# Kernel tuning notes

Hardware: AMD Instinct MI355X
Metric: run time of the kernel (lower is better)

## Reference

```python
import jax, jax.numpy as jnp
import numpy as np

N = 50000      # nodes
E = 800000     # edges (before self-loops)
F_IN = 128     # num_node_features
H = 128        # hidden_channels
G = 256        # graphs in batch
T = 4          # num_tasks


def setup_inputs() -> dict:
    key = jax.random.key(0)
    ks = jax.random.split(key, 12)
    x = jax.random.normal(ks[0], (N, F_IN), jnp.float32)
    edge_index = jax.random.randint(ks[1], (2, E), 0, N, dtype=jnp.int64)
    batch = jnp.sort(jax.random.randint(ks[2], (N,), 0, G, dtype=jnp.int64))
    s_in = 1.0 / np.sqrt(F_IN)
    s_h = 1.0 / np.sqrt(H)
    W1 = jax.random.normal(ks[3], (F_IN, H), jnp.float32) * s_in
    b1 = jnp.zeros((H,), jnp.float32)
    W2 = jax.random.normal(ks[4], (H, H), jnp.float32) * s_h
    b2 = jnp.zeros((H,), jnp.float32)
    Wfc = jax.random.normal(ks[5], (H, H), jnp.float32) * s_h
    bfc = jnp.zeros((H,), jnp.float32)
    Wh = jax.random.normal(ks[6], (T, H, 2), jnp.float32) * s_h
    bh = jnp.zeros((T, 2), jnp.float32)
    return {"x": x, "edge_index": edge_index, "batch": batch,
            "W1": W1, "b1": b1, "W2": W2, "b2": b2,
            "Wfc": Wfc, "bfc": bfc, "Wh": Wh, "bh": bh}


def _gcn_layer(x, W, b, src, dst, dinv):
    # GCNConv: out = D^{-1/2}(A+I)D^{-1/2} X W + b  (self-loops already in src/dst)
    h = x @ W                                    # [N, H] dense transform first (fewer edge features)
    coef = dinv[src] * dinv[dst]                 # [E+N] symmetric normalization
    msg = h[src] * coef[:, None]                 # [E+N, H] gathered messages
    out = jax.ops.segment_sum(msg, dst, num_segments=N)
    return out + b


def reference(x, edge_index, batch, W1, b1, W2, b2, Wfc, bfc, Wh, bh):
    loops = jnp.arange(N, dtype=edge_index.dtype)
    src = jnp.concatenate([edge_index[0], loops])  # [E+N]
    dst = jnp.concatenate([edge_index[1], loops])
    deg = jax.ops.segment_sum(jnp.ones_like(dst, dtype=x.dtype), dst, num_segments=N)
    dinv = jax.lax.rsqrt(deg)                      # deg >= 1 due to self-loops

    h = jax.nn.relu(_gcn_layer(x, W1, b1, src, dst, dinv))
    h = jax.nn.relu(_gcn_layer(h, W2, b2, src, dst, dinv))

    # global_mean_pool over batch ids
    sums = jax.ops.segment_sum(h, batch, num_segments=G)          # [G, H]
    cnt = jax.ops.segment_sum(jnp.ones((N,), h.dtype), batch, num_segments=G)
    pooled = sums / jnp.maximum(cnt, 1.0)[:, None]

    z = jax.nn.relu(pooled @ Wfc + bfc)                           # [G, H]
    out = jnp.einsum('gh,thc->tgc', z, Wh) + bh[:, None, :]       # [T, G, 2]
    return out
```

## Files before the change

### kernel.cpp

```cpp
#include <hip/hip_runtime.h>
#include <math.h>

constexpr int N = 50000;
constexpr int E = 800000;
constexpr int F = 128;
constexpr int G = 256;
constexpr int T = 4;

constexpr int BSH   = 5;
constexpr int BNODES= 1 << BSH;
constexpr int NBUCK = (N + BNODES - 1) / BNODES;
constexpr int CHUNK = 2048;
constexpr int NCHUNK= (E + CHUNK - 1) / CHUNK;
constexpr int SSH   = 13;

constexpr int WC_BLKS  = (F * F + 255) / 256;
constexpr int PRE_H0   = 2 * WC_BLKS;
constexpr int PRE_BLKS = PRE_H0 + NCHUNK;

constexpr int GB1 = (N + 63) / 64;
constexpr int AGB = N / 16;

typedef __attribute__((ext_vector_type(8))) short short8;
typedef __attribute__((ext_vector_type(4))) float floatx4;

__device__ inline float bf2f(unsigned short u) {
    union { unsigned int i; float f; } v;
    v.i = ((unsigned int)u) << 16;
    return v.f;
}
__device__ inline unsigned short f2bf(float f) {
    union { float f; unsigned int i; } v;
    v.f = f;
    unsigned int r = v.i + 0x7FFF + ((v.i >> 16) & 1);
    return (unsigned short)(r >> 16);
}
__device__ inline unsigned int pack2bf(float a, float b) {
    return (unsigned int)f2bf(a) | ((unsigned int)f2bf(b) << 16);
}

__device__ inline void wcast_one(const float* __restrict__ W,
                                 unsigned short* __restrict__ Whi,
                                 unsigned short* __restrict__ Wlo, int i) {
    if (i >= F * F) return;
    int k = i >> 7, n = i & 127;
    float w = W[i];
    unsigned short hi = f2bf(w);
    unsigned short lo = f2bf(w - bf2f(hi));
    int s = k >> 5, q = (k >> 3) & 3, j = k & 7;
    int idx = (((s * 128 + n) * 4 + q) * 8) + j;
    Whi[idx] = hi;
    Wlo[idx] = lo;
}

__global__ __launch_bounds__(256) void k_pre(const float* __restrict__ W1, const float* __restrict__ W2,
                                             unsigned short* __restrict__ w1h, unsigned short* __restrict__ w1l,
                                             unsigned short* __restrict__ w2h, unsigned short* __restrict__ w2l,
                                             const int* __restrict__ dst, int* __restrict__ cnts) {
    __shared__ int h[NBUCK];
    int b = blockIdx.x, t = threadIdx.x;
    if (b < WC_BLKS) {
        wcast_one(W1, w1h, w1l, b * 256 + t);
    } else if (b < 2 * WC_BLKS) {
        wcast_one(W2, w2h, w2l, (b - WC_BLKS) * 256 + t);
    } else {
        int chunk = b - PRE_H0;
        for (int i = t; i < NBUCK; i += 256) h[i] = 0;
        __syncthreads();
        int base = chunk * CHUNK;
        for (int i = t; i < CHUNK; i += 256) {
            int e = base + i;
            if (e < E) atomicAdd(&h[dst[e] >> BSH], 1);
        }
        __syncthreads();
        for (int i = t; i < NBUCK; i += 256) cnts[chunk * NBUCK + i] = h[i];
    }
}

__global__ __launch_bounds__(256) void k_colscan(int* __restrict__ cnts, int* __restrict__ btot) {
    int j = blockIdx.x * 256 + threadIdx.x;
    if (j >= NBUCK) return;
    int run = 0;
    for (int k = 0; k < NCHUNK; ++k) {
        int v = cnts[k * NBUCK + j];
        cnts[k * NBUCK + j] = run;
        run += v;
    }
    btot[j] = run;
}

__global__ __launch_bounds__(256) void k_bucketscan(const int* __restrict__ btot,
                                                    int* __restrict__ bucketbase) {
    __shared__ int part[256];
    int t = threadIdx.x;
    constexpr int CH = (NBUCK + 255) / 256;
    int beg = t * CH;
    int end = (beg + CH < NBUCK) ? beg + CH : NBUCK;
    int tot[CH];
    int s = 0;
    for (int i = beg; i < end; ++i) {
        tot[i - beg] = btot[i];
        s += btot[i];
    }
    part[t] = s;
    __syncthreads();
    for (int off = 1; off < 256; off <<= 1) {
        int u = (t >= off) ? part[t - off] : 0;
        __syncthreads();
        part[t] += u;
        __syncthreads();
    }
    int run = (t == 0) ? 0 : part[t - 1];
    for (int i = beg; i < end; ++i) {
        bucketbase[i] = run;
        run += tot[i - beg];
    }
    if (t == 255) bucketbase[NBUCK] = part[255];
}

__global__ __launch_bounds__(256) void k_fillb(const int* __restrict__ src,
                                               const int* __restrict__ dst,
                                               const int* __restrict__ cnts,
                                               const int* __restrict__ bucketbase,
                                               unsigned int* __restrict__ staging) {
    __shared__ int lofs[NBUCK];
    int chunk = blockIdx.x, t = threadIdx.x;
    for (int i = t; i < NBUCK; i += 256)
        lofs[i] = bucketbase[i] + cnts[chunk * NBUCK + i];
    __syncthreads();
    int base = chunk * CHUNK;
    for (int i = t; i < CHUNK; i += 256) {
        int e = base + i;
        if (e < E) {
            int d = dst[e];
            int pos = atomicAdd(&lofs[d >> BSH], 1);
            staging[pos] = (unsigned int)src[e] | ((unsigned int)(d & (BNODES - 1)) << 16);
        }
    }
}

__global__ __launch_bounds__(256) void k_passB(const unsigned int* __restrict__ staging,
                                               const int* __restrict__ bucketbase,
                                               int* __restrict__ csr,
                                               int* __restrict__ rowstart,
                                               float* __restrict__ dinv) {
    __shared__ unsigned int ent[1024];
    __shared__ int h[BNODES * 8], off_a[BNODES * 8];
    __shared__ int nodebase[BNODES], ndeg[BNODES];
    int b = blockIdx.x, t = threadIdx.x;
    int jb = bucketbase[b], je = bucketbase[b + 1];
    int M = je - jb;
    if (M > 1024) M = 1024;
    if (t < BNODES * 8) h[t] = 0;
    __syncthreads();

    for (int i = t; i < M; i += 256) {
        unsigned int en = staging[jb + i];
        ent[i] = en;
        int key = (((en >> 16) & (BNODES - 1)) << 3) | ((en & 0xFFFFu) >> SSH);
        atomicAdd(&h[key], 1);
    }
    __syncthreads();

    if (t < BNODES) {
        int s = 0;
#pragma unroll
        for (int c = 0; c < 8; ++c) s += h[t * 8 + c];
        ndeg[t] = s;
    }
    __syncthreads();
    if (t == 0) {
        int run = jb;
        for (int k = 0; k < BNODES; ++k) {
            nodebase[k] = run;
            run += ndeg[k];
        }
    }
    __syncthreads();
    if (t < BNODES) {
        int run = nodebase[t];
#pragma unroll
        for (int c = 0; c < 8; ++c) {
            off_a[t * 8 + c] = run;
            run += h[t * 8 + c];
        }
        int node = b * BNODES + t;
        if (node < N) {
            rowstart[node] = nodebase[t];
            dinv[node] = rsqrtf((float)(ndeg[t] + 1));
        }
    }
    if (b == 0 && t == 0) rowstart[N] = E;
    __syncthreads();

    for (int i = t; i < M; i += 256) {
        unsigned int en = ent[i];
        int key = (((en >> 16) & (BNODES - 1)) << 3) | ((en & 0xFFFFu) >> SSH);
        int loc = atomicAdd(&off_a[key], 1);
        csr[loc] = (int)(en & 0xFFFFu);
    }
}

template <bool ABF16>
__device__ __forceinline__ void gemm_body(const void* __restrict__ Ain,
                                          const unsigned short* __restrict__ Wph,
                                          const unsigned short* __restrict__ Wpl,
                                          const float* __restrict__ dinv,
                                          unsigned short* __restrict__ C16,
                                          int row0, int tid) {
    __shared__ __align__(16) unsigned short Albs[64 * 136];

    if (ABF16) {
        const uint4* A8 = (const uint4*)Ain;
        for (int f = tid; f < 64 * 16; f += 256) {
            int r = f >> 4, kq = f & 15;
            int row = row0 + r;
            uint4 v = make_uint4(0u, 0u, 0u, 0u);
            if (row < N) v = A8[row * 16 + kq];
            *(uint4*)&Albs[r * 136 + kq * 8] = v;
        }
    } else {
        const float4* A4 = (const float4*)Ain;
        for (int f = tid; f < 64 * 32; f += 256) {
            int r = f >> 5, kq = f & 31;
            int row = row0 + r;
            float4 v = make_float4(0.f, 0.f, 0.f, 0.f);
            if (row < N) v = A4[row * 32 + kq];
            ushort4 o;
            o.x = f2bf(v.x); o.y = f2bf(v.y); o.z = f2bf(v.z); o.w = f2bf(v.w);
            *(ushort4*)&Albs[r * 136 + kq * 4] = o;
        }
    }
    __syncthreads();

    int wv = tid >> 6;
    int lane = tid & 63;
    int c16 = lane & 15;
    int q = lane >> 4;
    int m = wv * 16 + c16;

    floatx4 acc[8];
#pragma unroll
    for (int nt = 0; nt < 8; ++nt) acc[nt] = (floatx4){0.f, 0.f, 0.f, 0.f};

    const short8* WH = (const short8*)Wph;
    const short8* WL = (const short8*)Wpl;
#pragma unroll
    for (int s = 0; s < 4; ++s) {
        short8 a = *(const short8*)&Albs[m * 136 + s * 32 + q * 8];
        int wb = s * 512 + c16 * 4 + q;
#pragma unroll
        for (int nt = 0; nt < 8; ++nt) {
            acc[nt] = __builtin_amdgcn_mfma_f32_16x16x32_bf16(a, WH[wb + nt * 64], acc[nt], 0, 0, 0);
            acc[nt] = __builtin_amdgcn_mfma_f32_16x16x32_bf16(a, WL[wb + nt * 64], acc[nt], 0, 0, 0);
        }
    }

    int rbase = row0 + wv * 16 + q * 4;
#pragma unroll
    for (int r = 0; r < 4; ++r) {
        int row = rbase + r;
        if (row < N) {
            float dv = dinv[row];
#pragma unroll
            for (int nt = 0; nt < 8; ++nt)
                C16[row * 128 + nt * 16 + c16] = f2bf(acc[nt][r] * dv);
        }
    }
}

template <bool ABF16>
__global__ __launch_bounds__(256) void k_gemm(const void* __restrict__ Ain,
                                              const unsigned short* __restrict__ Wph,
                                              const unsigned short* __restrict__ Wpl,
                                              const float* __restrict__ dinv,
                                              unsigned short* __restrict__ C16) {
    gemm_body<ABF16>(Ain, Wph, Wpl, dinv, C16, blockIdx.x * 64, threadIdx.x);
}

__device__ inline void fma8(const uint4& u, float c, float* acc) {
    union { unsigned int i; float f; } a;
    a.i = u.x << 16;          acc[0] = fmaf(a.f, c, acc[0]);
    a.i = u.x & 0xFFFF0000u;  acc[1] = fmaf(a.f, c, acc[1]);
    a.i = u.y << 16;          acc[2] = fmaf(a.f, c, acc[2]);
    a.i = u.y & 0xFFFF0000u;  acc[3] = fmaf(a.f, c, acc[3]);
    a.i = u.z << 16;          acc[4] = fmaf(a.f, c, acc[4]);
    a.i = u.z & 0xFFFF0000u;  acc[5] = fmaf(a.f, c, acc[5]);
    a.i = u.w << 16;          acc[6] = fmaf(a.f, c, acc[6]);
    a.i = u.w & 0xFFFF0000u;  acc[7] = fmaf(a.f, c, acc[7]);
}

__device__ __forceinline__ void agg_loop(const uint4* __restrict__ t8,
                                         const int* __restrict__ csr,
                                         int jb, int je, int lane, float* acc) {
    for (int j = jb; j < je; j += 8) {
        int e[8];
        float msk[8];
#pragma unroll
        for (int k = 0; k < 8; ++k) {
            int idx = j + k;
            e[k] = csr[idx < je ? idx : je - 1];
            msk[k] = (idx < je) ? 1.0f : 0.0f;
        }
        uint4 u[8];
#pragma unroll
        for (int k = 0; k < 8; ++k) u[k] = t8[e[k] * 16 + lane];
#pragma unroll
        for (int k = 0; k < 8; ++k) fma8(u[k], msk[k], acc);
    }
}

__global__ __launch_bounds__(256) void k_agg1gemm(const unsigned short* __restrict__ tmp16,
                                                  const int* __restrict__ csr,
                                                  const int* __restrict__ rowstart,
                                                  const float* __restrict__ dinv,
                                                  const float* __restrict__ bias,
                                                  const unsigned short* __restrict__ w2h,
                                                  const unsigned short* __restrict__ w2l,
                                                  unsigned short* __restrict__ tmp2) {
    __shared__ __align__(16) unsigned short Albs[16 * 136];
    int tid = threadIdx.x;
    int row0 = blockIdx.x * 16;

    {
        int node = row0 + (tid >> 4);
        int lane = tid & 15;
        const uint4* t8 = (const uint4*)tmp16;
        float acc[8] = {0.f, 0.f, 0.f, 0.f, 0.f, 0.f, 0.f, 0.f};
        fma8(t8[node * 16 + lane], 1.0f, acc);
        agg_loop(t8, csr, rowstart[node], rowstart[node + 1], lane, acc);

        float di = dinv[node];
        const float4* b4 = (const float4*)bias;
        float4 ba = b4[lane * 2], bb = b4[lane * 2 + 1];
        uint4 o;
        o.x = pack2bf(fmaxf(fmaf(acc[0], di, ba.x), 0.f), fmaxf(fmaf(acc[1], di, ba.y), 0.f));
        o.y = pack2bf(fmaxf(fmaf(acc[2], di, ba.z), 0.f), fmaxf(fmaf(acc[3], di, ba.w), 0.f));
        o.z = pack2bf(fmaxf(fmaf(acc[4], di, bb.x), 0.f), fmaxf(fmaf(acc[5], di, bb.y), 0.f));
        o.w = pack2bf(fmaxf(fmaf(acc[6], di, bb.z), 0.f), fmaxf(fmaf(acc[7], di, bb.w), 0.f));
        *(uint4*)&Albs[(tid >> 4) * 136 + lane * 8] = o;
    }
    __syncthreads();

    int wv = tid >> 6;
    int lane = tid & 63;
    int c16 = lane & 15;
    int q = lane >> 4;

    floatx4 acc[2];
    acc[0] = (floatx4){0.f, 0.f, 0.f, 0.f};
    acc[1] = (floatx4){0.f, 0.f, 0.f, 0.f};

    const short8* WH = (const short8*)w2h;
    const short8* WL = (const short8*)w2l;
#pragma unroll
    for (int s = 0; s < 4; ++s) {
        short8 a = *(const short8*)&Albs[c16 * 136 + s * 32 + q * 8];
        int wb = s * 512 + c16 * 4 + q;
#pragma unroll
        for (int i = 0; i < 2; ++i) {
            int nt = wv * 2 + i;
            acc[i] = __builtin_amdgcn_mfma_f32_16x16x32_bf16(a, WH[wb + nt * 64], acc[i], 0, 0, 0);
            acc[i] = __builtin_amdgcn_mfma_f32_16x16x32_bf16(a, WL[wb + nt * 64], acc[i], 0, 0, 0);
        }
    }

    int rbase = row0 + q * 4;
#pragma unroll
    for (int r = 0; r < 4; ++r) {
        int row = rbase + r;
        float dv = dinv[row];
#pragma unroll
        for (int i = 0; i < 2; ++i) {
            int nt = wv * 2 + i;
            tmp2[row * 128 + nt * 16 + c16] = f2bf(acc[i][r] * dv);
        }
    }
}

__global__ __launch_bounds__(256) void k_agg(const unsigned short* __restrict__ tmp16,
                                             const int* __restrict__ csr,
                                             const int* __restrict__ rowstart,
                                             const float* __restrict__ dinv,
                                             const float* __restrict__ bias,
                                             unsigned short* __restrict__ out16) {
    int node = (blockIdx.x * blockDim.x + threadIdx.x) >> 4;
    int lane = threadIdx.x & 15;
    if (node >= N) return;
    const uint4* t8 = (const uint4*)tmp16;
    float acc[8] = {0.f, 0.f, 0.f, 0.f, 0.f, 0.f, 0.f, 0.f};
    fma8(t8[node * 16 + lane], 1.0f, acc);
    agg_loop(t8, csr, rowstart[node], rowstart[node + 1], lane, acc);

    float di = dinv[node];
    const float4* b4 = (const float4*)bias;
    float4 ba = b4[lane * 2], bb = b4[lane * 2 + 1];
    uint4 o;
    o.x = pack2bf(fmaxf(fmaf(acc[0], di, ba.x), 0.f), fmaxf(fmaf(acc[1], di, ba.y), 0.f));
    o.y = pack2bf(fmaxf(fmaf(acc[2], di, ba.z), 0.f), fmaxf(fmaf(acc[3], di, ba.w), 0.f));
    o.z = pack2bf(fmaxf(fmaf(acc[4], di, bb.x), 0.f), fmaxf(fmaf(acc[5], di, bb.y), 0.f));
    o.w = pack2bf(fmaxf(fmaf(acc[6], di, bb.z), 0.f), fmaxf(fmaf(acc[7], di, bb.w), 0.f));
    ((uint4*)out16)[node * 16 + lane] = o;
}

__global__ __launch_bounds__(256) void k_poolhead(const unsigned short* __restrict__ h16,
                                                  const int* __restrict__ batch,
                                                  const float* __restrict__ Wfc,
                                                  const float* __restrict__ bfc,
                                                  const float* __restrict__ Wh,
                                                  const float* __restrict__ bh,
                                                  float* __restrict__ out) {
    __shared__ float red[16][128];
    __shared__ float p[128];
    __shared__ float zs[128];
    int g = blockIdx.x, t = threadIdx.x;
    int rg = t >> 4, lane = t & 15;

    int lo = 0, hi = N;
    while (lo < hi) { int m = (lo + hi) >> 1; if (batch[m] < g) lo = m + 1; else hi = m; }
    int lo1 = lo, hi1 = N;
    while (lo1 < hi1) { int m = (lo1 + hi1) >> 1; if (batch[m] < g + 1) lo1 = m + 1; else hi1 = m; }
    int cnt = lo1 - lo;

    float acc[8] = {0.f, 0.f, 0.f, 0.f, 0.f, 0.f, 0.f, 0.f};
    const uint4* h4 = (const uint4*)h16;
    for (int i = lo + rg; i < lo1; i += 16)
        fma8(h4[i * 16 + lane], 1.0f, acc);
#pragma unroll
    for (int k = 0; k < 8; ++k) red[rg][lane * 8 + k] = acc[k];
    __syncthreads();

    if (t < 128) {
        float s = 0.f;
#pragma unroll
        for (int r = 0; r < 16; ++r) s += red[r][t];
        p[t] = s / (float)((cnt > 1) ? cnt : 1);
    }
    __syncthreads();

    if (t < 128) {
        float a = bfc[t];
        for (int k = 0; k < F; ++k) a = fmaf(p[k], Wfc[k * F + t], a);
        zs[t] = fmaxf(a, 0.f);
    }
    __syncthreads();

    if (t < T * 2) {
        int task = t >> 1, c = t & 1;
        float a = bh[task * 2 + c];
        const float* wr = &Wh[task * F * 2 + c];
        for (int h = 0; h < F; ++h) a = fmaf(zs[h], wr[h * 2], a);
        out[task * (G * 2) + g * 2 + c] = a;
    }
}

extern "C" void kernel_launch(void* const* d_in, const int* in_sizes, int n_in,
                              void* d_out, int out_size, void* d_ws, size_t ws_size,
                              hipStream_t stream) {
    const float* x    = (const float*)d_in[0];
    const int*   ei   = (const int*)d_in[1];
    const int*   batch= (const int*)d_in[2];
    const float* W1   = (const float*)d_in[3];
    const float* b1   = (const float*)d_in[4];
    const float* W2   = (const float*)d_in[5];
    const float* b2   = (const float*)d_in[6];
    const float* Wfc  = (const float*)d_in[7];
    const float* bfc  = (const float*)d_in[8];
    const float* Wh   = (const float*)d_in[9];
    const float* bh   = (const float*)d_in[10];
    float* out = (float*)d_out;

    const int* srcp = ei;
    const int* dstp = ei + E;

    char* w = (char*)d_ws;
    auto alloc = [&](size_t bytes) {
        char* p = w;
        w += (bytes + 255) & ~(size_t)255;
        return p;
    };
    unsigned short* tmp16 = (unsigned short*)alloc((size_t)N * F * 2);
    unsigned short* tmp2  = (unsigned short*)alloc((size_t)N * F * 2);
    unsigned short* hbuf16= (unsigned short*)alloc((size_t)N * F * 2);
    int*   csr      = (int*)  alloc((size_t)E * 4);
    unsigned int* staging = (unsigned int*)alloc((size_t)E * 4);
    int*   cnts     = (int*)  alloc((size_t)NCHUNK * NBUCK * 4);
    int*   btot     = (int*)  alloc((size_t)NBUCK * 4);
    int*   bucketbase=(int*)  alloc((size_t)(NBUCK + 1) * 4);
    int*   rowstart = (int*)  alloc((size_t)(N + 1) * 4);
    float* dinv     = (float*)alloc((size_t)N * 4);
    unsigned short* w1h = (unsigned short*)alloc((size_t)F * F * 2);
    unsigned short* w1l = (unsigned short*)alloc((size_t)F * F * 2);
    unsigned short* w2h = (unsigned short*)alloc((size_t)F * F * 2);
    unsigned short* w2l = (unsigned short*)alloc((size_t)F * F * 2);

    k_pre<<<PRE_BLKS, 256, 0, stream>>>(W1, W2, w1h, w1l, w2h, w2l, dstp, cnts);

    k_colscan<<<(NBUCK + 255) / 256, 256, 0, stream>>>(cnts, btot);
    k_bucketscan<<<1, 256, 0, stream>>>(btot, bucketbase);
    k_fillb<<<NCHUNK, 256, 0, stream>>>(srcp, dstp, cnts, bucketbase, staging);
    k_passB<<<NBUCK, 256, 0, stream>>>(staging, bucketbase, csr, rowstart, dinv);

    k_gemm<false><<<GB1, 256, 0, stream>>>(x, w1h, w1l, dinv, tmp16);

    k_agg1gemm<<<AGB, 256, 0, stream>>>(tmp16, csr, rowstart, dinv, b1, w2h, w2l, tmp2);

    k_agg<<<(N * 16 + 255) / 256, 256, 0, stream>>>(tmp2, csr, rowstart, dinv, b2, hbuf16);

    k_poolhead<<<G, 256, 0, stream>>>(hbuf16, batch, Wfc, bfc, Wh, bh, out);
}
```

Baseline: 246.6 us.

## Fuse mean-pool into aggregation, merge column scan with first GEMM, per-edge dinv

Removes the dinv scaling from the GEMM epilogues and instead applies dinv[src] per edge inside the aggregation loop. This lets the first GEMM run before the CSR build, so it is merged with a parallel per-bucket column scan into one launch. The second aggregation now pools directly into a zeroed G×F buffer via shared-memory run-length reduction and atomics, which eliminates the hbuf16 write and re-read and one kernel launch. The trade-off is an extra per-edge dinv gather and float atomics that make summation order nondeterministic.

```diff
diff --git a/kernel.cpp b/kernel.cpp
--- a/kernel.cpp
+++ b/kernel.cpp
@@ -15,10 +15,13 @@
 constexpr int SSH   = 13;
 
 constexpr int WC_BLKS  = (F * F + 255) / 256;
-constexpr int PRE_H0   = 2 * WC_BLKS;
+constexpr int PRE_Z0   = 2 * WC_BLKS;
+constexpr int PRE_ZB   = (G * F + 255) / 256;
+constexpr int PRE_H0   = PRE_Z0 + PRE_ZB;
 constexpr int PRE_BLKS = PRE_H0 + NCHUNK;
 
 constexpr int GB1 = (N + 63) / 64;
+constexpr int GCB = GB1 + NBUCK;
 constexpr int AGB = N / 16;
 
 typedef __attribute__((ext_vector_type(8))) short short8;
@@ -56,13 +59,16 @@
 __global__ __launch_bounds__(256) void k_pre(const float* __restrict__ W1, const float* __restrict__ W2,
                                              unsigned short* __restrict__ w1h, unsigned short* __restrict__ w1l,
                                              unsigned short* __restrict__ w2h, unsigned short* __restrict__ w2l,
-                                             const int* __restrict__ dst, int* __restrict__ cnts) {
+                                             const int* __restrict__ dst, int* __restrict__ cnts,
+                                             float* __restrict__ pooled) {
     __shared__ int h[NBUCK];
     int b = blockIdx.x, t = threadIdx.x;
     if (b < WC_BLKS) {
         wcast_one(W1, w1h, w1l, b * 256 + t);
     } else if (b < 2 * WC_BLKS) {
         wcast_one(W2, w2h, w2l, (b - WC_BLKS) * 256 + t);
+    } else if (b < PRE_H0) {
+        pooled[(b - PRE_Z0) * 256 + t] = 0.f;
     } else {
         int chunk = b - PRE_H0;
         for (int i = t; i < NBUCK; i += 256) h[i] = 0;
@@ -75,18 +81,6 @@
         __syncthreads();
         for (int i = t; i < NBUCK; i += 256) cnts[chunk * NBUCK + i] = h[i];
     }
-}
-
-__global__ __launch_bounds__(256) void k_colscan(int* __restrict__ cnts, int* __restrict__ btot) {
-    int j = blockIdx.x * 256 + threadIdx.x;
-    if (j >= NBUCK) return;
-    int run = 0;
-    for (int k = 0; k < NCHUNK; ++k) {
-        int v = cnts[k * NBUCK + j];
-        cnts[k * NBUCK + j] = run;
-        run += v;
-    }
-    btot[j] = run;
 }
 
 __global__ __launch_bounds__(256) void k_bucketscan(const int* __restrict__ btot,
@@ -205,11 +199,9 @@
 __device__ __forceinline__ void gemm_body(const void* __restrict__ Ain,
                                           const unsigned short* __restrict__ Wph,
                                           const unsigned short* __restrict__ Wpl,
-                                          const float* __restrict__ dinv,
                                           unsigned short* __restrict__ C16,
-                                          int row0, int tid) {
-    __shared__ __align__(16) unsigned short Albs[64 * 136];
-
+                                          int row0, int tid,
+                                          unsigned short* __restrict__ Albs) {
     if (ABF16) {
         const uint4* A8 = (const uint4*)Ain;
         for (int f = tid; f < 64 * 16; f += 256) {
@@ -261,21 +253,43 @@
     for (int r = 0; r < 4; ++r) {
         int row = rbase + r;
         if (row < N) {
-            float dv = dinv[row];
 #pragma unroll
             for (int nt = 0; nt < 8; ++nt)
-                C16[row * 128 + nt * 16 + c16] = f2bf(acc[nt][r] * dv);
-        }
-    }
-}
-
-template <bool ABF16>
-__global__ __launch_bounds__(256) void k_gemm(const void* __restrict__ Ain,
-                                              const unsigned short* __restrict__ Wph,
-                                              const unsigned short* __restrict__ Wpl,
-                                              const float* __restrict__ dinv,
-                                              unsigned short* __restrict__ C16) {
-    gemm_body<ABF16>(Ain, Wph, Wpl, dinv, C16, blockIdx.x * 64, threadIdx.x);
+                C16[row * 128 + nt * 16 + c16] = f2bf(acc[nt][r]);
+        }
+    }
+}
+
+__global__ __launch_bounds__(256) void k_gemmcol(const float* __restrict__ x,
+                                                 const unsigned short* __restrict__ w1h,
+                                                 const unsigned short* __restrict__ w1l,
+                                                 unsigned short* __restrict__ tmp16,
+                                                 int* __restrict__ cnts,
+                                                 int* __restrict__ btot) {
+    __shared__ __align__(16) unsigned short Albs[64 * 136];
+    int b = blockIdx.x, t = threadIdx.x;
+    if (b < GB1) {
+        gemm_body<false>(x, w1h, w1l, tmp16, b * 64, t, Albs);
+        return;
+    }
+    int j = b - GB1;
+    int* part = (int*)Albs;
+    int k0 = 2 * t, k1 = 2 * t + 1;
+    int v0 = (k0 < NCHUNK) ? cnts[k0 * NBUCK + j] : 0;
+    int v1 = (k1 < NCHUNK) ? cnts[k1 * NBUCK + j] : 0;
+    int s = v0 + v1;
+    part[t] = s;
+    __syncthreads();
+    for (int off = 1; off < 256; off <<= 1) {
+        int u = (t >= off) ? part[t - off] : 0;
+        __syncthreads();
+        part[t] += u;
+        __syncthreads();
+    }
+    int excl = part[t] - s;
+    if (k0 < NCHUNK) cnts[k0 * NBUCK + j] = excl;
+    if (k1 < NCHUNK) cnts[k1 * NBUCK + j] = excl + v0;
+    if (t == 255) btot[j] = part[255];
 }
 
 __device__ inline void fma8(const uint4& u, float c, float* acc) {
@@ -292,21 +306,22 @@
 
 __device__ __forceinline__ void agg_loop(const uint4* __restrict__ t8,
                                          const int* __restrict__ csr,
+                                         const float* __restrict__ dinv,
                                          int jb, int je, int lane, float* acc) {
     for (int j = jb; j < je; j += 8) {
         int e[8];
-        float msk[8];
+        float cf[8];
 #pragma unroll
         for (int k = 0; k < 8; ++k) {
             int idx = j + k;
             e[k] = csr[idx < je ? idx : je - 1];
-            msk[k] = (idx < je) ? 1.0f : 0.0f;
+            cf[k] = (idx < je) ? dinv[e[k]] : 0.0f;
         }
         uint4 u[8];
 #pragma unroll
         for (int k = 0; k < 8; ++k) u[k] = t8[e[k] * 16 + lane];
 #pragma unroll
-        for (int k = 0; k < 8; ++k) fma8(u[k], msk[k], acc);
+        for (int k = 0; k < 8; ++k) fma8(u[k], cf[k], acc);
     }
 }
 
@@ -326,11 +341,11 @@
         int node = row0 + (tid >> 4);
         int lane = tid & 15;
         const uint4* t8 = (const uint4*)tmp16;
+        float di = dinv[node];
         float acc[8] = {0.f, 0.f, 0.f, 0.f, 0.f, 0.f, 0.f, 0.f};
-        fma8(t8[node * 16 + lane], 1.0f, acc);
-        agg_loop(t8, csr, rowstart[node], rowstart[node + 1], lane, acc);
-
-        float di = dinv[node];
+        fma8(t8[node * 16 + lane], di, acc);
+        agg_loop(t8, csr, dinv, rowstart[node], rowstart[node + 1], lane, acc);
+
         const float4* b4 = (const float4*)bias;
         float4 ba = b4[lane * 2], bb = b4[lane * 2 + 1];
         uint4 o;
@@ -369,11 +384,10 @@
 #pragma unroll
     for (int r = 0; r < 4; ++r) {
         int row = rbase + r;
-        float dv = dinv[row];
 #pragma unroll
         for (int i = 0; i < 2; ++i) {
             int nt = wv * 2 + i;
-            tmp2[row * 128 + nt * 16 + c16] = f2bf(acc[i][r] * dv);
+            tmp2[row * 128 + nt * 16 + c16] = f2bf(acc[i][r]);
         }
     }
 }
@@ -383,74 +397,81 @@
                                              const int* __restrict__ rowstart,
                                              const float* __restrict__ dinv,
                                              const float* __restrict__ bias,
-                                             unsigned short* __restrict__ out16) {
-    int node = (blockIdx.x * blockDim.x + threadIdx.x) >> 4;
-    int lane = threadIdx.x & 15;
-    if (node >= N) return;
+                                             const int* __restrict__ batch,
+                                             float* __restrict__ pooled) {
+    __shared__ float red[16][128];
+    __shared__ int gid[16];
+    int tid = threadIdx.x;
+    int node0 = blockIdx.x * 16;
+    int ns = tid >> 4, lane = tid & 15;
+    int node = node0 + ns;
     const uint4* t8 = (const uint4*)tmp16;
+    float di = dinv[node];
     float acc[8] = {0.f, 0.f, 0.f, 0.f, 0.f, 0.f, 0.f, 0.f};
-    fma8(t8[node * 16 + lane], 1.0f, acc);
-    agg_loop(t8, csr, rowstart[node], rowstart[node + 1], lane, acc);
-
-    float di = dinv[node];
+    fma8(t8[node * 16 + lane], di, acc);
+    agg_loop(t8, csr, dinv, rowstart[node], rowstart[node + 1], lane, acc);
+
     const float4* b4 = (const float4*)bias;
     float4 ba = b4[lane * 2], bb = b4[lane * 2 + 1];
-    uint4 o;
-    o.x = pack2bf(fmaxf(fmaf(acc[0], di, ba.x), 0.f), fmaxf(fmaf(acc[1], di, ba.y), 0.f));
-    o.y = pack2bf(fmaxf(fmaf(acc[2], di, ba.z), 0.f), fmaxf(fmaf(acc[3], di, ba.w), 0.f));
-    o.z = pack2bf(fmaxf(fmaf(acc[4], di, bb.x), 0.f), fmaxf(fmaf(acc[5], di, bb.y), 0.f));
-    o.w = pack2bf(fmaxf(fmaf(acc[6], di, bb.z), 0.f), fmaxf(fmaf(acc[7], di, bb.w), 0.f));
-    ((uint4*)out16)[node * 16 + lane] = o;
-}
-
-__global__ __launch_bounds__(256) void k_poolhead(const unsigned short* __restrict__ h16,
+    red[ns][lane * 8 + 0] = fmaxf(fmaf(acc[0], di, ba.x), 0.f);
+    red[ns][lane * 8 + 1] = fmaxf(fmaf(acc[1], di, ba.y), 0.f);
+    red[ns][lane * 8 + 2] = fmaxf(fmaf(acc[2], di, ba.z), 0.f);
+    red[ns][lane * 8 + 3] = fmaxf(fmaf(acc[3], di, ba.w), 0.f);
+    red[ns][lane * 8 + 4] = fmaxf(fmaf(acc[4], di, bb.x), 0.f);
+    red[ns][lane * 8 + 5] = fmaxf(fmaf(acc[5], di, bb.y), 0.f);
+    red[ns][lane * 8 + 6] = fmaxf(fmaf(acc[6], di, bb.z), 0.f);
+    red[ns][lane * 8 + 7] = fmaxf(fmaf(acc[7], di, bb.w), 0.f);
+    if (tid < 16) gid[tid] = batch[node0 + tid];
+    __syncthreads();
+
+    if (tid < 128) {
+        int f = tid;
+        float run = 0.f;
+        int g = gid[0];
+        for (int r = 0; r < 16; ++r) {
+            if (gid[r] != g) {
+                atomicAdd(&pooled[g * 128 + f], run);
+                run = 0.f;
+                g = gid[r];
+            }
+            run += red[r][f];
+        }
+        atomicAdd(&pooled[g * 128 + f], run);
+    }
+}
+
+__global__ __launch_bounds__(128) void k_poolhead(const float* __restrict__ pooled,
                                                   const int* __restrict__ batch,
                                                   const float* __restrict__ Wfc,
                                                   const float* __restrict__ bfc,
                                                   const float* __restrict__ Wh,
                                                   const float* __restrict__ bh,
                                                   float* __restrict__ out) {
-    __shared__ float red[16][128];
     __shared__ float p[128];
     __shared__ float zs[128];
     int g = blockIdx.x, t = threadIdx.x;
-    int rg = t >> 4, lane = t & 15;
 
     int lo = 0, hi = N;
     while (lo < hi) { int m = (lo + hi) >> 1; if (batch[m] < g) lo = m + 1; else hi = m; }
     int lo1 = lo, hi1 = N;
     while (lo1 < hi1) { int m = (lo1 + hi1) >> 1; if (batch[m] < g + 1) lo1 = m + 1; else hi1 = m; }
     int cnt = lo1 - lo;
-
-    float acc[8] = {0.f, 0.f, 0.f, 0.f, 0.f, 0.f, 0.f, 0.f};
-    const uint4* h4 = (const uint4*)h16;
-    for (int i = lo + rg; i < lo1; i += 16)
-        fma8(h4[i * 16 + lane], 1.0f, acc);
-#pragma unroll
-    for (int k = 0; k < 8; ++k) red[rg][lane * 8 + k] = acc[k];
-    __syncthreads();
-
-    if (t < 128) {
-        float s = 0.f;
-#pragma unroll
-        for (int r = 0; r < 16; ++r) s += red[r][t];
-        p[t] = s / (float)((cnt > 1) ? cnt : 1);
-    }
-    __syncthreads();
-
-    if (t < 128) {
-        float a = bfc[t];
-        for (int k = 0; k < F; ++k) a = fmaf(p[k], Wfc[k * F + t], a);
-        zs[t] = fmaxf(a, 0.f);
-    }
+    float inv = 1.0f / (float)((cnt > 1) ? cnt : 1);
+
+    p[t] = pooled[g * 128 + t] * inv;
+    __syncthreads();
+
+    float a = bfc[t];
+    for (int k = 0; k < F; ++k) a = fmaf(p[k], Wfc[k * F + t], a);
+    zs[t] = fmaxf(a, 0.f);
     __syncthreads();
 
     if (t < T * 2) {
         int task = t >> 1, c = t & 1;
-        float a = bh[task * 2 + c];
+        float a2 = bh[task * 2 + c];
         const float* wr = &Wh[task * F * 2 + c];
-        for (int h = 0; h < F; ++h) a = fmaf(zs[h], wr[h * 2], a);
-        out[task * (G * 2) + g * 2 + c] = a;
+        for (int h = 0; h < F; ++h) a2 = fmaf(zs[h], wr[h * 2], a2);
+        out[task * (G * 2) + g * 2 + c] = a2;
     }
 }
 
@@ -481,7 +502,6 @@
     };
     unsigned short* tmp16 = (unsigned short*)alloc((size_t)N * F * 2);
     unsigned short* tmp2  = (unsigned short*)alloc((size_t)N * F * 2);
-    unsigned short* hbuf16= (unsigned short*)alloc((size_t)N * F * 2);
     int*   csr      = (int*)  alloc((size_t)E * 4);
     unsigned int* staging = (unsigned int*)alloc((size_t)E * 4);
     int*   cnts     = (int*)  alloc((size_t)NCHUNK * NBUCK * 4);
@@ -489,23 +509,23 @@
     int*   bucketbase=(int*)  alloc((size_t)(NBUCK + 1) * 4);
     int*   rowstart = (int*)  alloc((size_t)(N + 1) * 4);
     float* dinv     = (float*)alloc((size_t)N * 4);
+    float* pooled   = (float*)alloc((size_t)G * F * 4);
     unsigned short* w1h = (unsigned short*)alloc((size_t)F * F * 2);
     unsigned short* w1l = (unsigned short*)alloc((size_t)F * F * 2);
     unsigned short* w2h = (unsigned short*)alloc((size_t)F * F * 2);
     unsigned short* w2l = (unsigned short*)alloc((size_t)F * F * 2);
 
-    k_pre<<<PRE_BLKS, 256, 0, stream>>>(W1, W2, w1h, w1l, w2h, w2l, dstp, cnts);
-
-    k_colscan<<<(NBUCK + 255) / 256, 256, 0, stream>>>(cnts, btot);
+    k_pre<<<PRE_BLKS, 256, 0, stream>>>(W1, W2, w1h, w1l, w2h, w2l, dstp, cnts, pooled);
+
+    k_gemmcol<<<GCB, 256, 0, stream>>>(x, w1h, w1l, tmp16, cnts, btot);
+
     k_bucketscan<<<1, 256, 0, stream>>>(btot, bucketbase);
     k_fillb<<<NCHUNK, 256, 0, stream>>>(srcp, dstp, cnts, bucketbase, staging);
     k_passB<<<NBUCK, 256, 0, stream>>>(staging, bucketbase, csr, rowstart, dinv);
 
-    k_gemm<false><<<GB1, 256, 0, stream>>>(x, w1h, w1l, dinv, tmp16);
-
     k_agg1gemm<<<AGB, 256, 0, stream>>>(tmp16, csr, rowstart, dinv, b1, w2h, w2l, tmp2);
 
-    k_agg<<<(N * 16 + 255) / 256, 256, 0, stream>>>(tmp2, csr, rowstart, dinv, b2, hbuf16);
-
-    k_poolhead<<<G, 256, 0, stream>>>(hbuf16, batch, Wfc, bfc, Wh, bh, out);
-}
+    k_agg<<<AGB, 256, 0, stream>>>(tmp2, csr, rowstart, dinv, b2, batch, pooled);
+
+    k_poolhead<<<G, 128, 0, stream>>>(pooled, batch, Wfc, bfc, Wh, bh, out);
+}
```

Result: faster. 232.0 us (-5.9%).
